# Optimization experiments

Hardware: AMD Instinct MI355X
Metric: run time of the kernel (lower is better)

The kernel has to match this reference:

```python
import jax, jax.numpy as jnp
import numpy as np
from jax import lax

RES = 14
DIM = 384
KEY_DIM = 32
NUM_HEADS = 12
ATTN_RATIO = 4
NH_KD = KEY_DIM * NUM_HEADS            # 384
DH = ATTN_RATIO * KEY_DIM * NUM_HEADS  # 1536
HQKV = DH + 2 * NH_KD                  # 2304
BN_EPS = 1e-5


def _bias_idxs():
    ys, xs = np.meshgrid(np.arange(RES), np.arange(RES), indexing='ij')
    ys = ys.reshape(-1); xs = xs.reshape(-1)
    dy = np.abs(ys[:, None] - ys[None, :])
    dx = np.abs(xs[:, None] - xs[None, :])
    return jnp.asarray(dy * RES + dx, dtype=jnp.int32)  # [196,196], 196 unique offsets


def setup_inputs() -> dict:
    key = jax.random.key(0)
    ks = jax.random.split(key, 16)
    B = 128
    x = jax.random.normal(ks[0], (B, DIM, RES, RES), dtype=jnp.float32)
    # qkv: 1x1 conv DIM->HQKV + BN
    qkv_w = jax.random.normal(ks[1], (HQKV, DIM, 1, 1), dtype=jnp.float32) * 0.05
    qkv_g = jax.random.normal(ks[2], (HQKV,), dtype=jnp.float32) * 0.1 + 1.0
    qkv_b = jax.random.normal(ks[3], (HQKV,), dtype=jnp.float32) * 0.1
    qkv_m = jax.random.normal(ks[4], (HQKV,), dtype=jnp.float32) * 0.1
    qkv_v = jax.random.uniform(ks[5], (HQKV,), dtype=jnp.float32) + 0.5
    # dw: depthwise 3x3 conv on q channels + BN
    dw_w = jax.random.normal(ks[6], (NH_KD, 1, 3, 3), dtype=jnp.float32) * 0.2
    dw_g = jax.random.normal(ks[7], (NH_KD,), dtype=jnp.float32) * 0.1 + 1.0
    dw_b = jax.random.normal(ks[8], (NH_KD,), dtype=jnp.float32) * 0.1
    dw_m = jax.random.normal(ks[9], (NH_KD,), dtype=jnp.float32) * 0.1
    dw_v = jax.random.uniform(ks[10], (NH_KD,), dtype=jnp.float32) + 0.5
    # proj: ReLU -> 1x1 conv DH->DIM + BN
    proj_w = jax.random.normal(ks[11], (DIM, DH, 1, 1), dtype=jnp.float32) * 0.05
    proj_g = jax.random.normal(ks[12], (DIM,), dtype=jnp.float32) * 0.1 + 1.0
    proj_b = jax.random.normal(ks[13], (DIM,), dtype=jnp.float32) * 0.1
    proj_m = jax.random.normal(ks[14], (DIM,), dtype=jnp.float32) * 0.1
    proj_v = jax.random.uniform(ks[15], (DIM,), dtype=jnp.float32) + 0.5
    ab = jax.random.normal(jax.random.fold_in(key, 99), (NUM_HEADS, RES * RES), dtype=jnp.float32) * 0.1
    return {
        'x': x,
        'qkv_w': qkv_w, 'qkv_g': qkv_g, 'qkv_b': qkv_b, 'qkv_m': qkv_m, 'qkv_v': qkv_v,
        'dw_w': dw_w, 'dw_g': dw_g, 'dw_b': dw_b, 'dw_m': dw_m, 'dw_v': dw_v,
        'proj_w': proj_w, 'proj_g': proj_g, 'proj_b': proj_b, 'proj_m': proj_m, 'proj_v': proj_v,
        'attn_biases': ab,
        'bias_idxs': _bias_idxs(),
    }


def _bn(x, g, b, m, v):
    scale = g / jnp.sqrt(v + BN_EPS)
    return x * scale[None, :, None, None] + (b - m * scale)[None, :, None, None]


def reference(x, qkv_w, qkv_g, qkv_b, qkv_m, qkv_v,
              dw_w, dw_g, dw_b, dw_m, dw_v,
              proj_w, proj_g, proj_b, proj_m, proj_v,
              attn_biases, bias_idxs):
    B, _, H, W = x.shape
    n = H * W
    scale = KEY_DIM ** -0.5
    # 1x1 conv + BN
    qkv = jnp.einsum('bchw,oc->bohw', x, qkv_w[:, :, 0, 0])
    qkv = _bn(qkv, qkv_g, qkv_b, qkv_m, qkv_v)
    q = qkv[:, :NH_KD]
    k = qkv[:, NH_KD:2 * NH_KD]
    v = qkv[:, 2 * NH_KD:]
    # depthwise 3x3 conv + BN on q
    q = lax.conv_general_dilated(q, dw_w, (1, 1), ((1, 1), (1, 1)),
                                 dimension_numbers=('NCHW', 'OIHW', 'NCHW'),
                                 feature_group_count=NH_KD)
    q = _bn(q, dw_g, dw_b, dw_m, dw_v)
    # heads: [b, h, d, n]
    q = q.reshape(B, NUM_HEADS, KEY_DIM, n)
    k = k.reshape(B, NUM_HEADS, KEY_DIM, n)
    v = v.reshape(B, NUM_HEADS, ATTN_RATIO * KEY_DIM, n)
    bias = attn_biases[:, bias_idxs]  # [h, n, n]
    attn = jnp.einsum('bhdn,bhdm->bhnm', q, k) * scale + bias[None]
    attn = jax.nn.softmax(attn, axis=-1)
    out = jnp.einsum('bhdm,bhnm->bhdn', v, attn).reshape(B, DH, H, W)
    out = jax.nn.relu(out)
    out = jnp.einsum('bchw,oc->bohw', out, proj_w[:, :, 0, 0])
    return _bn(out, proj_g, proj_b, proj_m, proj_v)
```

## Files before the change

kernel.cpp:

```cpp
#include <hip/hip_runtime.h>

typedef __bf16 bf16;
typedef bf16 bf16x8 __attribute__((ext_vector_type(8)));
typedef bf16 bf16x4 __attribute__((ext_vector_type(4)));
typedef short short4v __attribute__((ext_vector_type(4)));
typedef float f32x4 __attribute__((ext_vector_type(4)));

#define NPIX 196
#define CIN 384
#define NHEADS 12
#define MPAD 224
#define VSTRIDE 232
#define OSTRIDE 40
#define TSTRIDE 136

__device__ __forceinline__ float ldf(const void* p, size_t i, int f) {
    return f ? ((const float*)p)[i] : (float)((const bf16*)p)[i];
}

__device__ __forceinline__ void gld16(const void* g, void* lds_wave_base) {
    __builtin_amdgcn_global_load_lds(
        (const __attribute__((address_space(1))) void*)(unsigned long long)g,
        (__attribute__((address_space(3))) void*)(unsigned long long)lds_wave_base,
        16, 0, 0);
}

__device__ __forceinline__ int xcd_swizzle(int orig, int nwg) {
    int q = nwg >> 3, r = nwg & 7;
    int xcd = orig & 7, idx = orig >> 3;
    return (xcd < r ? xcd * (q + 1) : r * (q + 1) + (xcd - r) * q) + idx;
}

__device__ __forceinline__ f32x4 mfma16(bf16x4 a, bf16x4 b, f32x4 c) {
#if __has_builtin(__builtin_amdgcn_mfma_f32_16x16x16bf16_1k)
    return __builtin_amdgcn_mfma_f32_16x16x16bf16_1k(
        __builtin_bit_cast(short4v, a), __builtin_bit_cast(short4v, b), c, 0, 0, 0);
#else
    asm volatile("v_mfma_f32_16x16x16_bf16 %0, %1, %2, %0" : "+v"(c) : "v"(a), "v"(b));
    return c;
#endif
}

__device__ __forceinline__ f32x4 vmax4(f32x4 a, f32x4 b) {
    f32x4 r;
    r[0] = fmaxf(a[0], b[0]);
    r[1] = fmaxf(a[1], b[1]);
    r[2] = fmaxf(a[2], b[2]);
    r[3] = fmaxf(a[3], b[3]);
    return r;
}

__global__ void detect_kernel(const unsigned int* __restrict__ x, int* __restrict__ flag) {
    __shared__ int cnt;
    if (threadIdx.x == 0) cnt = 0;
    __syncthreads();
    int c = 0;
#pragma unroll
    for (int k = 0; k < 8; k++) {
        unsigned int w = x[threadIdx.x * 8 + k];
        unsigned int e = (w >> 7) & 0xFFu;
        if (e > 200u) c++;
    }
    atomicAdd(&cnt, c);
    __syncthreads();
    if (threadIdx.x == 0) *flag = (cnt >= 16) ? 1 : 0;
}

__global__ void convert_kernel(const void* __restrict__ src, bf16* __restrict__ dst, int n,
                               const int* __restrict__ flag) {
    int f = *flag;
    for (int i = blockIdx.x * 256 + threadIdx.x; i < n; i += gridDim.x * 256)
        dst[i] = (bf16)ldf(src, i, f);
}

__global__ void transpose_x_kernel(const void* __restrict__ x, const int* __restrict__ flag,
                                   bf16* __restrict__ xt, int b0) {
    __shared__ bf16 tile[32][33];
    int f = *flag;
    int b = blockIdx.z, gb = b0 + b;
    int c0 = blockIdx.y * 32;
    int hw0 = blockIdx.x * 32;
    int tx = threadIdx.x, ty = threadIdx.y;
    int hw = hw0 + tx, c = c0 + ty;
    if (hw < NPIX) tile[ty][tx] = (bf16)ldf(x, ((size_t)gb * CIN + c) * NPIX + hw, f);
    __syncthreads();
    int hw2 = hw0 + ty, c2 = c0 + tx;
    if (hw2 < NPIX) xt[((size_t)b * NPIX + hw2) * CIN + c2] = tile[tx][ty];
}

__device__ __forceinline__ void gemm_tile(const bf16* __restrict__ A, const bf16* __restrict__ B,
                                          int K, bf16* smem, f32x4 acc[4][4]) {
    int tid = threadIdx.x;
    int wave = tid >> 6, lane = tid & 63;
    int wm = wave >> 1, wn = wave & 1;
    int row = lane & 15, grp = lane >> 4;
    int sr = lane >> 3;
    int scg = (lane & 7) ^ sr;
    const int BUF = 128 * 64;
    bf16* As = smem;
    bf16* Bs = smem + 2 * BUF;
    const bf16* Ag = A + (size_t)(wave * 8 + sr) * K + scg * 8;
    const bf16* Bg = B + (size_t)(wave * 8 + sr) * K + scg * 8;
#pragma unroll
    for (int p = 0; p < 4; p++) {
        gld16(Ag + (size_t)(p * 32) * K, As + (p * 256 + wave * 64) * 8);
        gld16(Bg + (size_t)(p * 32) * K, Bs + (p * 256 + wave * 64) * 8);
    }
    int cur = 0;
#pragma unroll 1
    for (int kb = 0; kb < K; kb += 64) {
        if (kb + 64 < K) {
            bf16* Asn = As + (cur ^ 1) * BUF;
            bf16* Bsn = Bs + (cur ^ 1) * BUF;
#pragma unroll
            for (int p = 0; p < 4; p++) {
                gld16(Ag + (size_t)(p * 32) * K + kb + 64, Asn + (p * 256 + wave * 64) * 8);
                gld16(Bg + (size_t)(p * 32) * K + kb + 64, Bsn + (p * 256 + wave * 64) * 8);
            }
            __builtin_amdgcn_sched_barrier(0);
            asm volatile("s_waitcnt vmcnt(8)" ::: "memory");
        } else {
            __builtin_amdgcn_sched_barrier(0);
            asm volatile("s_waitcnt vmcnt(0)" ::: "memory");
        }
        __builtin_amdgcn_s_barrier();
        __builtin_amdgcn_sched_barrier(0);
        const bf16* Asc = As + cur * BUF;
        const bf16* Bsc = Bs + cur * BUF;
#pragma unroll
        for (int ki = 0; ki < 2; ki++) {
            bf16x8 af[4], bfr[4];
#pragma unroll
            for (int t = 0; t < 4; t++) {
                int ra = wm * 64 + t * 16 + row;
                af[t] = *(const bf16x8*)(Asc + ra * 64 + (((ki * 4 + grp) ^ (ra & 7)) * 8));
                int rb = wn * 64 + t * 16 + row;
                bfr[t] = *(const bf16x8*)(Bsc + rb * 64 + (((ki * 4 + grp) ^ (rb & 7)) * 8));
            }
#pragma unroll
            for (int mt = 0; mt < 4; mt++)
#pragma unroll
                for (int nt = 0; nt < 4; nt++)
                    acc[mt][nt] =
                        __builtin_amdgcn_mfma_f32_16x16x32_bf16(af[mt], bfr[nt], acc[mt][nt], 0, 0, 0);
        }
        __builtin_amdgcn_sched_barrier(0);
        __builtin_amdgcn_s_barrier();
        cur ^= 1;
    }
    __builtin_amdgcn_sched_barrier(0);
}

__global__ __launch_bounds__(256) void gemm_qkv_kernel(
    const bf16* __restrict__ xt, const bf16* __restrict__ w,
    const void* __restrict__ g, const void* __restrict__ bb,
    const void* __restrict__ mm, const void* __restrict__ vv, const int* __restrict__ flag,
    bf16* __restrict__ qb, bf16* __restrict__ kt, bf16* __restrict__ vb) {
    __shared__ bf16 smem[4 * 128 * 64];
    f32x4 acc[4][4];
#pragma unroll
    for (int i = 0; i < 4; i++)
#pragma unroll
        for (int j = 0; j < 4; j++) acc[i][j] = (f32x4){0.f, 0.f, 0.f, 0.f};
    int nwg = gridDim.x * gridDim.y;
    int l = xcd_swizzle(blockIdx.y * gridDim.x + blockIdx.x, nwg);
    int m0 = (l % gridDim.x) * 128, n0 = (l / gridDim.x) * 128;
    gemm_tile(w + (size_t)m0 * CIN, xt + (size_t)n0 * CIN, CIN, smem, acc);
    int f = *flag;
    int tid = threadIdx.x;
    int wave = tid >> 6, lane = tid & 63;
    int wm = wave >> 1, wn = wave & 1, row = lane & 15, grp = lane >> 4;
    if (m0 >= 384 && m0 < 768) {
        bf16* tbuf = smem;
#pragma unroll
        for (int mt = 0; mt < 4; mt++) {
#pragma unroll
            for (int r = 0; r < 4; r++) {
                int ol = wm * 64 + mt * 16 + grp * 4 + r;
                int o = m0 + ol;
                float scv = ldf(g, o, f) * rsqrtf(ldf(vv, o, f) + 1e-5f);
                float sh = ldf(bb, o, f) - ldf(mm, o, f) * scv;
#pragma unroll
                for (int nt = 0; nt < 4; nt++) {
                    int nl = wn * 64 + nt * 16 + row;
                    tbuf[nl * TSTRIDE + ol] = (bf16)(acc[mt][nt][r] * scv + sh);
                }
            }
        }
        __syncthreads();
#pragma unroll
        for (int it = 0; it < 8; it++) {
            int g2 = it * 256 + tid;
            int nl = g2 >> 4, ch = g2 & 15;
            *(bf16x8*)(kt + (size_t)(n0 + nl) * CIN + (m0 - 384) + ch * 8) =
                *(const bf16x8*)(tbuf + nl * TSTRIDE + ch * 8);
        }
    } else {
#pragma unroll
        for (int mt = 0; mt < 4; mt++) {
#pragma unroll
            for (int r = 0; r < 4; r++) {
                int o = m0 + wm * 64 + mt * 16 + grp * 4 + r;
                float scv = ldf(g, o, f) * rsqrtf(ldf(vv, o, f) + 1e-5f);
                float sh = ldf(bb, o, f) - ldf(mm, o, f) * scv;
#pragma unroll
                for (int nt = 0; nt < 4; nt++) {
                    int n = n0 + wn * 64 + nt * 16 + row;
                    int b = n / NPIX, hw = n - b * NPIX;
                    float val = acc[mt][nt][r] * scv + sh;
                    bf16 bv = (bf16)val;
                    if (o < 384) {
                        qb[((size_t)b * 384 + o) * NPIX + hw] = bv;
                    } else {
                        vb[((size_t)b * 1536 + (o - 768)) * MPAD + hw] = bv;
                    }
                }
            }
        }
    }
}

__global__ __launch_bounds__(256) void gemm_proj_kernel(
    const bf16* __restrict__ ot, const bf16* __restrict__ w,
    const void* __restrict__ g, const void* __restrict__ bb,
    const void* __restrict__ mm, const void* __restrict__ vv, const int* __restrict__ flag,
    void* __restrict__ out, int b0) {
    __shared__ bf16 smem[4 * 128 * 64];
    f32x4 acc[4][4];
#pragma unroll
    for (int i = 0; i < 4; i++)
#pragma unroll
        for (int j = 0; j < 4; j++) acc[i][j] = (f32x4){0.f, 0.f, 0.f, 0.f};
    int nwg = gridDim.x * gridDim.y;
    int l = xcd_swizzle(blockIdx.y * gridDim.x + blockIdx.x, nwg);
    int m0 = (l % gridDim.x) * 128, n0 = (l / gridDim.x) * 128;
    gemm_tile(w + (size_t)m0 * 1536, ot + (size_t)n0 * 1536, 1536, smem, acc);
    int f = *flag;
    int wave = threadIdx.x >> 6, lane = threadIdx.x & 63;
    int wm = wave >> 1, wn = wave & 1, row = lane & 15, grp = lane >> 4;
#pragma unroll
    for (int mt = 0; mt < 4; mt++) {
#pragma unroll
        for (int r = 0; r < 4; r++) {
            int o = m0 + wm * 64 + mt * 16 + grp * 4 + r;
            float scv = ldf(g, o, f) * rsqrtf(ldf(vv, o, f) + 1e-5f);
            float sh = ldf(bb, o, f) - ldf(mm, o, f) * scv;
#pragma unroll
            for (int nt = 0; nt < 4; nt++) {
                int n = n0 + wn * 64 + nt * 16 + row;
                int b = n / NPIX, hw = n - b * NPIX;
                float val = acc[mt][nt][r] * scv + sh;
                size_t oidx = ((size_t)(b0 + b) * 384 + o) * NPIX + hw;
                if (f) ((float*)out)[oidx] = val;
                else ((bf16*)out)[oidx] = (bf16)val;
            }
        }
    }
}

__global__ void dwconv_kernel(const bf16* __restrict__ qb, const bf16* __restrict__ w,
                              const void* __restrict__ g, const void* __restrict__ bb,
                              const void* __restrict__ mm, const void* __restrict__ vv,
                              const int* __restrict__ flag, bf16* __restrict__ qt) {
    __shared__ bf16 tile[32][33];
    int f = *flag;
    int b = blockIdx.z;
    int c0 = blockIdx.y * 32, hw0 = blockIdx.x * 32;
    int tx = threadIdx.x, ty = threadIdx.y;
    int c = c0 + ty, hw = hw0 + tx;
    if (hw < NPIX) {
        int y = hw / 14, x = hw % 14;
        float acc = 0.f;
        const bf16* wp = w + c * 9;
        const bf16* qp = qb + ((size_t)b * 384 + c) * NPIX;
#pragma unroll
        for (int ky = 0; ky < 3; ky++) {
            int yy = y + ky - 1;
            if (yy < 0 || yy >= 14) continue;
#pragma unroll
            for (int kx = 0; kx < 3; kx++) {
                int xx = x + kx - 1;
                if (xx < 0 || xx >= 14) continue;
                acc += (float)qp[yy * 14 + xx] * (float)wp[ky * 3 + kx];
            }
        }
        float sc = ldf(g, c, f) * rsqrtf(ldf(vv, c, f) + 1e-5f);
        float sh = ldf(bb, c, f) - ldf(mm, c, f) * sc;
        tile[ty][tx] = (bf16)(acc * sc + sh);
    }
    __syncthreads();
    int hw2 = hw0 + ty, c2 = c0 + tx;
    if (hw2 < NPIX) qt[((size_t)b * NPIX + hw2) * CIN + c2] = tile[tx][ty];
}

__global__ void bias_gather_kernel(const void* __restrict__ ab, const int* __restrict__ idx,
                                   const int* __restrict__ flag, float* __restrict__ biasf) {
    int f = *flag;
    int t = blockIdx.x * 256 + threadIdx.x;
    if (t >= NHEADS * NPIX * MPAD) return;
    int h = t / (NPIX * MPAD);
    int rem = t - h * (NPIX * MPAD);
    int n = rem / MPAD, m = rem - n * MPAD;
    biasf[t] = (m < NPIX) ? ldf(ab, h * NPIX + idx[n * NPIX + m], f) : -1e30f;
}

__global__ void zero_vpad_kernel(bf16* __restrict__ vb, int rows) {
    int t = blockIdx.x * 256 + threadIdx.x;
    if (t >= rows * 7) return;
    int r = t / 7, c = t - r * 7;
    *(unsigned long long*)(vb + (size_t)r * MPAD + NPIX + c * 4) = 0ull;
}

__global__ __launch_bounds__(256, 2) void attn_kernel(
    const bf16* __restrict__ qt, const bf16* __restrict__ ktp, const bf16* __restrict__ vb,
    const float* __restrict__ biasf, bf16* __restrict__ ot) {
    __shared__ bf16 Vs[128 * VSTRIDE];
    __shared__ bf16 Osh[4][16 * OSTRIDE];
    int nwg = gridDim.x * gridDim.y;
    int l = xcd_swizzle(blockIdx.y * gridDim.x + blockIdx.x, nwg);
    int h = l % NHEADS, b = l / NHEADS;
    int tid = threadIdx.x;
    int wave = tid >> 6, lane = tid & 63;
    int row = lane & 15, grp = lane >> 4;
    const float scale = 0.17677669529663687f;
    const f32x4 zf = {0.f, 0.f, 0.f, 0.f};

    {
        const bf16* vsrc = vb + ((size_t)b * 1536 + h * 128) * MPAD;
#pragma unroll
        for (int it = 0; it < 14; it++) {
            int i = it * 256 + tid;
            int r = i / 28, gch = i - r * 28;
            *(bf16x8*)(Vs + r * VSTRIDE + gch * 8) = *(const bf16x8*)(vsrc + (size_t)i * 8);
        }
    }
    __syncthreads();

    const bf16* vls = Vs + row * VSTRIDE + grp * 4;

    for (int nb = wave; nb < 13; nb += 4) {
        int n0 = nb * 16;
        int n = n0 + row;
        int nc = n > 195 ? 195 : n;

        bf16x8 aq = *(const bf16x8*)(qt + ((size_t)b * NPIX + nc) * CIN + h * 32 + grp * 8);

        f32x4 sacc[14];
#pragma unroll
        for (int mt = 0; mt < 14; mt++) {
            int krow = mt * 16 + row;
            if (krow > 195) krow = 195;
            bf16x8 ak = *(const bf16x8*)(ktp + ((size_t)b * NPIX + krow) * CIN + h * 32 + grp * 8);
            sacc[mt] = __builtin_amdgcn_mfma_f32_16x16x32_bf16(ak, aq, zf, 0, 0, 0);
        }

        const float* bp = biasf + ((size_t)h * NPIX + nc) * MPAD + grp * 4;
        f32x4 mxv = {-3.4e38f, -3.4e38f, -3.4e38f, -3.4e38f};
#pragma unroll
        for (int mt = 0; mt < 14; mt++) {
            f32x4 bv = *(const f32x4*)(bp + mt * 16);
            f32x4 s = sacc[mt] * scale + bv;
            sacc[mt] = s;
            mxv = vmax4(mxv, s);
        }
        float mx = fmaxf(fmaxf(mxv[0], mxv[1]), fmaxf(mxv[2], mxv[3]));
        mx = fmaxf(mx, __shfl_xor(mx, 16));
        mx = fmaxf(mx, __shfl_xor(mx, 32));

        f32x4 sumv = zf;
        bf16x4 pf[14];
#pragma unroll
        for (int mt = 0; mt < 14; mt++) {
            f32x4 e;
#pragma unroll
            for (int r = 0; r < 4; r++) e[r] = __expf(sacc[mt][r] - mx);
            sumv += e;
            bf16x4 pb;
#pragma unroll
            for (int r = 0; r < 4; r++) pb[r] = (bf16)e[r];
            pf[mt] = pb;
        }
        float sum = (sumv[0] + sumv[1]) + (sumv[2] + sumv[3]);
        sum += __shfl_xor(sum, 16);
        sum += __shfl_xor(sum, 32);
        float inv = 1.f / sum;

        f32x4 oacc[8];
#pragma unroll
        for (int dt = 0; dt < 8; dt++) oacc[dt] = zf;
#pragma unroll
        for (int mt = 0; mt < 14; mt++) {
            bf16x4 p = pf[mt];
#pragma unroll
            for (int dt = 0; dt < 8; dt++) {
                bf16x4 v4 = *(const bf16x4*)(vls + dt * 16 * VSTRIDE + mt * 16);
                oacc[dt] = mfma16(v4, p, oacc[dt]);
            }
        }

        bf16* osw = Osh[wave];
        int r2 = lane >> 2, c2 = lane & 3;
        int n2 = n0 + r2;
        bf16* op = ot + ((size_t)b * NPIX + n2) * 1536 + h * 128;
#pragma unroll
        for (int dp = 0; dp < 4; dp++) {
#pragma unroll
            for (int u = 0; u < 2; u++) {
                int dt = dp * 2 + u;
                bf16x4 o4;
#pragma unroll
                for (int r = 0; r < 4; r++) {
                    float v = oacc[dt][r] * inv;
                    o4[r] = (bf16)(v > 0.f ? v : 0.f);
                }
                *(bf16x4*)(osw + row * OSTRIDE + u * 16 + grp * 4) = o4;
            }
            asm volatile("s_waitcnt lgkmcnt(0)" ::: "memory");
            if (n2 < NPIX) {
                bf16x8 ov = *(const bf16x8*)(osw + r2 * OSTRIDE + c2 * 8);
                *(bf16x8*)(op + dp * 32 + c2 * 8) = ov;
            }
            asm volatile("s_waitcnt lgkmcnt(0)" ::: "memory");
        }
    }
}

extern "C" void kernel_launch(void* const* d_in, const int* in_sizes, int n_in,
                              void* d_out, int out_size, void* d_ws, size_t ws_size,
                              hipStream_t stream) {
    const void* x      = d_in[0];
    const void* qkv_w  = d_in[1];
    const void* qkv_g  = d_in[2];
    const void* qkv_b  = d_in[3];
    const void* qkv_m  = d_in[4];
    const void* qkv_v  = d_in[5];
    const void* dw_w   = d_in[6];
    const void* dw_g   = d_in[7];
    const void* dw_b   = d_in[8];
    const void* dw_m   = d_in[9];
    const void* dw_v   = d_in[10];
    const void* proj_w = d_in[11];
    const void* proj_g = d_in[12];
    const void* proj_b = d_in[13];
    const void* proj_m = d_in[14];
    const void* proj_v = d_in[15];
    const void* ab     = d_in[16];
    const int*  idx    = (const int*)d_in[17];

    char* ws = (char*)d_ws;
    size_t off = 0;
    auto alloc = [&](size_t bytes) { void* p = ws + off; off += (bytes + 255) & ~(size_t)255; return p; };

    int*   flag = (int*)alloc(4);
    bf16*  wq   = (bf16*)alloc((size_t)2304 * 384 * 2);
    bf16*  wp   = (bf16*)alloc((size_t)384 * 1536 * 2);
    bf16*  wd   = (bf16*)alloc((size_t)384 * 9 * 2);
    float* biasf= (float*)alloc((size_t)NHEADS * NPIX * MPAD * 4);
    size_t fixed = off;

    const size_t s_xt = (size_t)NPIX * CIN;
    const size_t s_qb = (size_t)384 * NPIX;
    const size_t s_kt = (size_t)NPIX * 384;
    const size_t s_vb = (size_t)1536 * MPAD;
    const size_t s_ot = (size_t)NPIX * 1536;
    const size_t per_image = (s_xt + s_qb + s_kt + s_vb + s_ot) * 2;

    int CB = 128;
    while (CB > 32 && fixed + (size_t)CB * per_image > ws_size) CB >>= 1;

    bf16* xt  = (bf16*)alloc((size_t)CB * s_xt * 2);
    bf16* qb  = (bf16*)alloc((size_t)CB * s_qb * 2);
    bf16* ktp = (bf16*)alloc((size_t)CB * s_kt * 2);
    bf16* vb  = (bf16*)alloc((size_t)CB * s_vb * 2);
    bf16* ot  = (bf16*)alloc((size_t)CB * s_ot * 2);
    bf16* qt  = xt;

    detect_kernel<<<dim3(1), dim3(256), 0, stream>>>((const unsigned int*)x, flag);
    convert_kernel<<<dim3(256), dim3(256), 0, stream>>>(qkv_w, wq, 2304 * 384, flag);
    convert_kernel<<<dim3(256), dim3(256), 0, stream>>>(proj_w, wp, 384 * 1536, flag);
    convert_kernel<<<dim3(4), dim3(256), 0, stream>>>(dw_w, wd, 384 * 9, flag);
    int bg = (NHEADS * NPIX * MPAD + 255) / 256;
    bias_gather_kernel<<<dim3(bg), dim3(256), 0, stream>>>(ab, idx, flag, biasf);
    int vrows = CB * 1536;
    zero_vpad_kernel<<<dim3((vrows * 7 + 255) / 256), dim3(256), 0, stream>>>(vb, vrows);

    dim3 tb(32, 32);
    for (int b0 = 0; b0 < 128; b0 += CB) {
        int cb = (128 - b0 < CB) ? (128 - b0) : CB;
        int ntiles = (cb * NPIX) / 128;
        transpose_x_kernel<<<dim3(7, 12, cb), tb, 0, stream>>>(x, flag, xt, b0);
        gemm_qkv_kernel<<<dim3(18, ntiles), dim3(256), 0, stream>>>(xt, wq, qkv_g, qkv_b, qkv_m,
                                                                    qkv_v, flag, qb, ktp, vb);
        dwconv_kernel<<<dim3(7, 12, cb), tb, 0, stream>>>(qb, wd, dw_g, dw_b, dw_m, dw_v, flag, qt);
        attn_kernel<<<dim3(NHEADS, cb), dim3(256), 0, stream>>>(qt, ktp, vb, biasf, ot);
        gemm_proj_kernel<<<dim3(3, ntiles), dim3(256), 0, stream>>>(ot, wp, proj_g, proj_b, proj_m,
                                                                    proj_v, flag, d_out, b0);
    }
}
```

Baseline: 446.9 us.

## Load GEMM fragments directly from global memory into registers, dropping LDS staging

Replaces the LDS double-buffered global_load_lds GEMM tile with a register double-buffered scheme where each wave loads its MFMA operand fragments straight from global memory. This removes LDS traffic and the block barriers per K step, and frees shared memory for occupancy. In exchange each operand row is loaded by two waves (no sharing through LDS), global loads are less coalesced (16-byte chunks strided by K), and register pressure rises sharply with 32 bf16x8 fragment registers plus 64 accumulator registers.

```diff
diff --git a/kernel.cpp b/kernel.cpp
--- a/kernel.cpp
+++ b/kernel.cpp
@@ -16,13 +16,6 @@
 
 __device__ __forceinline__ float ldf(const void* p, size_t i, int f) {
     return f ? ((const float*)p)[i] : (float)((const bf16*)p)[i];
-}
-
-__device__ __forceinline__ void gld16(const void* g, void* lds_wave_base) {
-    __builtin_amdgcn_global_load_lds(
-        (const __attribute__((address_space(1))) void*)(unsigned long long)g,
-        (__attribute__((address_space(3))) void*)(unsigned long long)lds_wave_base,
-        16, 0, 0);
 }
 
 __device__ __forceinline__ int xcd_swizzle(int orig, int nwg) {
@@ -88,67 +81,41 @@
     if (hw2 < NPIX) xt[((size_t)b * NPIX + hw2) * CIN + c2] = tile[tx][ty];
 }
 
-__device__ __forceinline__ void gemm_tile(const bf16* __restrict__ A, const bf16* __restrict__ B,
-                                          int K, bf16* smem, f32x4 acc[4][4]) {
+template <int K>
+__device__ __forceinline__ void gemm_direct(const bf16* __restrict__ A, const bf16* __restrict__ B,
+                                            f32x4 acc[4][4]) {
     int tid = threadIdx.x;
     int wave = tid >> 6, lane = tid & 63;
     int wm = wave >> 1, wn = wave & 1;
     int row = lane & 15, grp = lane >> 4;
-    int sr = lane >> 3;
-    int scg = (lane & 7) ^ sr;
-    const int BUF = 128 * 64;
-    bf16* As = smem;
-    bf16* Bs = smem + 2 * BUF;
-    const bf16* Ag = A + (size_t)(wave * 8 + sr) * K + scg * 8;
-    const bf16* Bg = B + (size_t)(wave * 8 + sr) * K + scg * 8;
-#pragma unroll
-    for (int p = 0; p < 4; p++) {
-        gld16(Ag + (size_t)(p * 32) * K, As + (p * 256 + wave * 64) * 8);
-        gld16(Bg + (size_t)(p * 32) * K, Bs + (p * 256 + wave * 64) * 8);
-    }
-    int cur = 0;
+    const bf16* Ab = A + (size_t)(wm * 64 + row) * K + grp * 8;
+    const bf16* Bb = B + (size_t)(wn * 64 + row) * K + grp * 8;
+    bf16x8 a0[8], b0[8], a1[8], b1[8];
+#define LOADF(aa, bb, kb)                                                         \
+    {                                                                             \
+        _Pragma("unroll") for (int f_ = 0; f_ < 8; f_++) {                        \
+            int t_ = f_ & 3, ki_ = f_ >> 2;                                       \
+            aa[f_] = *(const bf16x8*)(Ab + (size_t)(t_ * 16) * K + (kb) + ki_ * 32); \
+            bb[f_] = *(const bf16x8*)(Bb + (size_t)(t_ * 16) * K + (kb) + ki_ * 32); \
+        }                                                                         \
+    }
+#define COMPF(aa, bb)                                                             \
+    _Pragma("unroll") for (int ki_ = 0; ki_ < 2; ki_++)                           \
+    _Pragma("unroll") for (int mt_ = 0; mt_ < 4; mt_++)                           \
+    _Pragma("unroll") for (int nt_ = 0; nt_ < 4; nt_++)                           \
+        acc[mt_][nt_] = __builtin_amdgcn_mfma_f32_16x16x32_bf16(                  \
+            aa[ki_ * 4 + mt_], bb[ki_ * 4 + nt_], acc[mt_][nt_], 0, 0, 0);
+
+    LOADF(a0, b0, 0);
 #pragma unroll 1
-    for (int kb = 0; kb < K; kb += 64) {
-        if (kb + 64 < K) {
-            bf16* Asn = As + (cur ^ 1) * BUF;
-            bf16* Bsn = Bs + (cur ^ 1) * BUF;
-#pragma unroll
-            for (int p = 0; p < 4; p++) {
-                gld16(Ag + (size_t)(p * 32) * K + kb + 64, Asn + (p * 256 + wave * 64) * 8);
-                gld16(Bg + (size_t)(p * 32) * K + kb + 64, Bsn + (p * 256 + wave * 64) * 8);
-            }
-            __builtin_amdgcn_sched_barrier(0);
-            asm volatile("s_waitcnt vmcnt(8)" ::: "memory");
-        } else {
-            __builtin_amdgcn_sched_barrier(0);
-            asm volatile("s_waitcnt vmcnt(0)" ::: "memory");
-        }
-        __builtin_amdgcn_s_barrier();
-        __builtin_amdgcn_sched_barrier(0);
-        const bf16* Asc = As + cur * BUF;
-        const bf16* Bsc = Bs + cur * BUF;
-#pragma unroll
-        for (int ki = 0; ki < 2; ki++) {
-            bf16x8 af[4], bfr[4];
-#pragma unroll
-            for (int t = 0; t < 4; t++) {
-                int ra = wm * 64 + t * 16 + row;
-                af[t] = *(const bf16x8*)(Asc + ra * 64 + (((ki * 4 + grp) ^ (ra & 7)) * 8));
-                int rb = wn * 64 + t * 16 + row;
-                bfr[t] = *(const bf16x8*)(Bsc + rb * 64 + (((ki * 4 + grp) ^ (rb & 7)) * 8));
-            }
-#pragma unroll
-            for (int mt = 0; mt < 4; mt++)
-#pragma unroll
-                for (int nt = 0; nt < 4; nt++)
-                    acc[mt][nt] =
-                        __builtin_amdgcn_mfma_f32_16x16x32_bf16(af[mt], bfr[nt], acc[mt][nt], 0, 0, 0);
-        }
-        __builtin_amdgcn_sched_barrier(0);
-        __builtin_amdgcn_s_barrier();
-        cur ^= 1;
-    }
-    __builtin_amdgcn_sched_barrier(0);
+    for (int kb = 0; kb < K; kb += 128) {
+        LOADF(a1, b1, kb + 64);
+        COMPF(a0, b0);
+        if (kb + 128 < K) LOADF(a0, b0, kb + 128);
+        COMPF(a1, b1);
+    }
+#undef LOADF
+#undef COMPF
 }
 
 __global__ __launch_bounds__(256) void gemm_qkv_kernel(
@@ -156,7 +123,7 @@
     const void* __restrict__ g, const void* __restrict__ bb,
     const void* __restrict__ mm, const void* __restrict__ vv, const int* __restrict__ flag,
     bf16* __restrict__ qb, bf16* __restrict__ kt, bf16* __restrict__ vb) {
-    __shared__ bf16 smem[4 * 128 * 64];
+    __shared__ bf16 tbuf[128 * TSTRIDE];
     f32x4 acc[4][4];
 #pragma unroll
     for (int i = 0; i < 4; i++)
@@ -165,13 +132,12 @@
     int nwg = gridDim.x * gridDim.y;
     int l = xcd_swizzle(blockIdx.y * gridDim.x + blockIdx.x, nwg);
     int m0 = (l % gridDim.x) * 128, n0 = (l / gridDim.x) * 128;
-    gemm_tile(w + (size_t)m0 * CIN, xt + (size_t)n0 * CIN, CIN, smem, acc);
+    gemm_direct<CIN>(w + (size_t)m0 * CIN, xt + (size_t)n0 * CIN, acc);
     int f = *flag;
     int tid = threadIdx.x;
     int wave = tid >> 6, lane = tid & 63;
     int wm = wave >> 1, wn = wave & 1, row = lane & 15, grp = lane >> 4;
     if (m0 >= 384 && m0 < 768) {
-        bf16* tbuf = smem;
 #pragma unroll
         for (int mt = 0; mt < 4; mt++) {
 #pragma unroll
@@ -225,7 +191,6 @@
     const void* __restrict__ g, const void* __restrict__ bb,
     const void* __restrict__ mm, const void* __restrict__ vv, const int* __restrict__ flag,
     void* __restrict__ out, int b0) {
-    __shared__ bf16 smem[4 * 128 * 64];
     f32x4 acc[4][4];
 #pragma unroll
     for (int i = 0; i < 4; i++)
@@ -234,7 +199,7 @@
     int nwg = gridDim.x * gridDim.y;
     int l = xcd_swizzle(blockIdx.y * gridDim.x + blockIdx.x, nwg);
     int m0 = (l % gridDim.x) * 128, n0 = (l / gridDim.x) * 128;
-    gemm_tile(w + (size_t)m0 * 1536, ot + (size_t)n0 * 1536, 1536, smem, acc);
+    gemm_direct<1536>(w + (size_t)m0 * 1536, ot + (size_t)n0 * 1536, acc);
     int f = *flag;
     int wave = threadIdx.x >> 6, lane = threadIdx.x & 63;
     int wm = wave >> 1, wn = wave & 1, row = lane & 15, grp = lane >> 4;
```

New measurement: 696.9 us. +56.0%, slower.
